# Kernel optimization log

Measured on AMD Instinct MI355X. Metric: run time of the kernel, lower is better.

Reference implementation:

```python
import jax, jax.numpy as jnp
import numpy as np
from jax import lax

B, N, D, OUT = 256, 4096, 512, 512
EPS = 1e-5
NPOINT = 128  # 4 modalities * 32 tokens each


def setup_inputs() -> dict:
    key = jax.random.key(0)
    ks = jax.random.split(key, 32)
    f32 = jnp.float32
    nrm = lambda k, s, sc=0.05: jax.random.normal(k, s, f32) * sc
    inp = {
        'rgb': jax.random.normal(ks[0], (B, 49, D), f32),
        'depth': jax.random.normal(ks[1], (B, 49, D), f32),
        'mmwave': jax.random.normal(ks[2], (B, 32, D), f32),
        'lidar': jax.random.normal(ks[3], (B, 32, D), f32),
        'lidar_points': jax.random.normal(ks[4], (B, N, 3), f32),
        # per-modality conv1d(k=1) weights, stacked [rgb, depth, mmwave, lidar]
        'conv_w': nrm(ks[5], (4, OUT, D)),
        'conv_b': nrm(ks[6], (4, OUT)),
        # eval-mode BatchNorm1d params per modality
        'bn_g': 1.0 + nrm(ks[7], (4, OUT)),
        'bn_b': nrm(ks[8], (4, OUT)),
        'bn_m': nrm(ks[9], (4, OUT)),
        'bn_v': 0.5 + jax.random.uniform(ks[10], (4, OUT), f32),
        # nn.Linear(49,32) for rgb/depth, nn.Linear(32,32) for mmwave/lidar
        'lin_w_img': nrm(ks[11], (2, 32, 49)),
        'lin_b_img': nrm(ks[12], (2, 32)),
        'lin_w_pc': nrm(ks[13], (2, 32, 32)),
        'lin_b_pc': nrm(ks[14], (2, 32)),
        # pos_enc_layer: Conv1d(3,128,1)+BN+ReLU, Conv1d(128,OUT,1)+BN+ReLU
        'pe_w1': nrm(ks[15], (128, 3)),
        'pe_b1': nrm(ks[16], (128,)),
        'pe_g1': 1.0 + nrm(ks[17], (128,)),
        'pe_bb1': nrm(ks[18], (128,)),
        'pe_m1': nrm(ks[19], (128,)),
        'pe_v1': 0.5 + jax.random.uniform(ks[20], (128,), f32),
        'pe_w2': nrm(ks[21], (OUT, 128)),
        'pe_b2': nrm(ks[22], (OUT,)),
        'pe_g2': 1.0 + nrm(ks[23], (OUT,)),
        'pe_bb2': nrm(ks[24], (OUT,)),
        'pe_m2': nrm(ks[25], (OUT,)),
        'pe_v2': 0.5 + jax.random.uniform(ks[26], (OUT,), f32),
    }
    return inp


def _bn(x, g, b, m, v):
    # x: [B, C, L]; eval-mode batchnorm over channel dim
    return (x - m[:, None]) * (g / jnp.sqrt(v + EPS))[:, None] + b[:, None]


def _branch(x, cw, cb, g, bb, m, v, lw, lb):
    # x: [B, L, D] (already the un-permuted feature); conv1d(k=1) == matmul
    h = jnp.einsum('bld,od->bol', x, cw) + cb[:, None]  # [B, OUT, L]
    h = jax.nn.relu(_bn(h, g, bb, m, v))
    h = jnp.einsum('bol,kl->bok', h, lw) + lb           # Linear on last dim -> [B, OUT, 32]
    return jax.nn.relu(h)


def _fps(xyz, npoint):
    # faithful farthest point sampling: npoint sequential iterations as lax.scan
    Bb, Nn, _ = xyz.shape
    far0 = jax.random.randint(jax.random.key(42), (Bb,), 0, Nn)
    dist0 = jnp.full((Bb, Nn), 1e10, xyz.dtype)
    def step(carry, _):
        distance, farthest = carry
        idx = jnp.broadcast_to(farthest[:, None, None], (Bb, 1, 3))
        centroid = jnp.take_along_axis(xyz, idx, axis=1)      # [B,1,3]
        d = jnp.sum((xyz - centroid) ** 2, -1)                # [B,N]
        distance = jnp.minimum(distance, d)
        return (distance, jnp.argmax(distance, -1)), farthest
    _, idxs = lax.scan(step, (dist0, far0), None, length=npoint)
    return jnp.transpose(idxs)  # [B, npoint]


def reference(rgb, depth, mmwave, lidar, lidar_points,
              conv_w, conv_b, bn_g, bn_b, bn_m, bn_v,
              lin_w_img, lin_b_img, lin_w_pc, lin_b_pc,
              pe_w1, pe_b1, pe_g1, pe_bb1, pe_m1, pe_v1,
              pe_w2, pe_b2, pe_g2, pe_bb2, pe_m2, pe_v2):
    # active_modalities = ['rgb','depth','mmwave','lidar']
    feats = [
        _branch(rgb,    conv_w[0], conv_b[0], bn_g[0], bn_b[0], bn_m[0], bn_v[0], lin_w_img[0], lin_b_img[0]),
        _branch(depth,  conv_w[1], conv_b[1], bn_g[1], bn_b[1], bn_m[1], bn_v[1], lin_w_img[1], lin_b_img[1]),
        _branch(mmwave, conv_w[2], conv_b[2], bn_g[2], bn_b[2], bn_m[2], bn_v[2], lin_w_pc[0], lin_b_pc[0]),
        _branch(lidar,  conv_w[3], conv_b[3], bn_g[3], bn_b[3], bn_m[3], bn_v[3], lin_w_pc[1], lin_b_pc[1]),
    ]
    proj = jnp.transpose(jnp.concatenate(feats, axis=2), (0, 2, 1))  # [B, 128, OUT]
    S = proj.shape[1]
    fps_idx = _fps(lidar_points, S)                                   # [B, S]
    gi = jnp.broadcast_to(fps_idx[..., None], (lidar_points.shape[0], S, 3))
    new_xyz = jnp.take_along_axis(lidar_points, gi, axis=1)           # [B, S, 3]
    h = jnp.einsum('bsd,od->bos', new_xyz, pe_w1) + pe_b1[:, None]    # [B,128,S]
    h = jax.nn.relu(_bn(h, pe_g1, pe_bb1, pe_m1, pe_v1))
    h = jnp.einsum('bcs,oc->bos', h, pe_w2) + pe_b2[:, None]          # [B,OUT,S]
    h = jax.nn.relu(_bn(h, pe_g2, pe_bb2, pe_m2, pe_v2))
    return proj + jnp.transpose(h, (0, 2, 1))
```

## Files before the change

kernel.cpp:

```cpp
#include <hip/hip_runtime.h>
#include <stdint.h>

typedef unsigned int u32;
typedef unsigned short u16;

typedef __attribute__((ext_vector_type(8))) short bf16x8;
typedef __attribute__((ext_vector_type(8))) unsigned short u16x8;
typedef __attribute__((ext_vector_type(4))) float f32x4;

__device__ __forceinline__ u16 f2bfu(float f) {
  union { float f; u32 u; } v; v.f = f;
  return (u16)((v.u + 0x7FFFu + ((v.u >> 16) & 1u)) >> 16);
}
__device__ __forceinline__ float bf2f(u16 h) {
  union { u32 u; float f; } v; v.u = ((u32)h) << 16;
  return v.f;
}

__device__ __forceinline__ void gload16(const void* g, void* l) {
  __builtin_amdgcn_global_load_lds(
      (const __attribute__((address_space(1))) void*)g,
      (__attribute__((address_space(3))) void*)l, 16, 0, 0);
}

// ... 16 lines not shown
                        x0 += x1; x1 = rotl32(x1,c); x1 ^= x0; \
                        x0 += x1; x1 = rotl32(x1,d); x1 ^= x0; }
  TF_G(13,15,26,6);  x0 += k1;  x1 += ks2 + 1u;
  TF_G(17,29,16,24); x0 += ks2; x1 += k0  + 2u;
  TF_G(13,15,26,6);  x0 += k0;  x1 += k1  + 3u;
  TF_G(17,29,16,24); x0 += k1;  x1 += ks2 + 4u;
  TF_G(13,15,26,6);  x0 += ks2; x1 += k0  + 5u;
#undef TF_G
  return make_uint2(x0, x1);
}

__global__ __launch_bounds__(256) void convert_kernel(
    const float* __restrict__ rgb, const float* __restrict__ depth,
    const float* __restrict__ mmw, const float* __restrict__ lid,
    const float* __restrict__ conv_w, u16* __restrict__ Wc, u16* __restrict__ Xc,
    const float* __restrict__ pw2,
    const float* __restrict__ pg1, const float* __restrict__ pbb1,
    const float* __restrict__ pm1, const float* __restrict__ pv1,
    const float* __restrict__ pb1,
    const float* __restrict__ pg2, const float* __restrict__ pbb2,
    const float* __restrict__ pm2, const float* __restrict__ pv2,
    const float* __restrict__ pb2,
    u16* __restrict__ W2h, u16* __restrict__ W2l,
    float* __restrict__ sc1C1, float* __restrict__ sc2C2)
{
  const int bid = blockIdx.x, tid = threadIdx.x;
  if (bid < 12288) {
    float4 v0 = make_float4(0.f, 0.f, 0.f, 0.f), v1 = v0;
    const int y = bid >> 4, ks = bid & 15;
    const int l = tid >> 2, seg = tid & 3;
    const float* xp; size_t row = 0; bool valid = true;
    if (y < 256)      { xp = rgb;   row = (size_t)y * 49 + l;         valid = (l < 49); }
    else if (y < 512) { xp = depth; row = (size_t)(y - 256) * 49 + l; valid = (l < 49); }
    else if (y < 640) { xp = mmw;   row = (size_t)(y - 512) * 64 + l; }
    else              { xp = lid;   row = (size_t)(y - 640) * 64 + l; }
    if (valid) {
      const float* s = xp + row * 512 + ks * 32 + seg * 8;
      v0 = *(const float4*)s; v1 = *(const float4*)(s + 4);
    }
    char* dst = (char*)Xc + (size_t)y * 65536 + ks * 4096 + l * 64 + ((seg ^ ((l >> 1) & 3)) << 4);
    u16x8 pk;
    pk[0] = f2bfu(v0.x); pk[1] = f2bfu(v0.y); pk[2] = f2bfu(v0.z); pk[3] = f2bfu(v0.w);
    pk[4] = f2bfu(v1.x); pk[5] = f2bfu(v1.y); pk[6] = f2bfu(v1.z); pk[7] = f2bfu(v1.w);
    *(u16x8*)dst = pk;
  } else if (bid < 12800) {
    const int t = bid - 12288;
    const int tile = t >> 1, half = t & 1;
    const int row = (tid >> 2) + half * 64, seg = tid & 3;
    const float* s = conv_w + (size_t)((tile >> 4) * 128 + row) * 512 + (tile & 15) * 32 + seg * 8;
    float4 v0 = *(const float4*)s; float4 v1 = *(const float4*)(s + 4);
    char* dst = (char*)Wc + (size_t)tile * 8192 + row * 64 + ((seg ^ ((row >> 1) & 3)) << 4);
    u16x8 pk;
    pk[0] = f2bfu(v0.x); pk[1] = f2bfu(v0.y); pk[2] = f2bfu(v0.z); pk[3] = f2bfu(v0.w);
    pk[4] = f2bfu(v1.x); pk[5] = f2bfu(v1.y); pk[6] = f2bfu(v1.z); pk[7] = f2bfu(v1.w);
    *(u16x8*)dst = pk;
  } else if (bid < 12832) {
    const int idx = (bid - 12800) * 2048 + tid * 8;
    const float* s = pw2 + idx;
    float4 v0 = *(const float4*)s; float4 v1 = *(const float4*)(s + 4);
    float vv[8] = {v0.x, v0.y, v0.z, v0.w, v1.x, v1.y, v1.z, v1.w};
    u16x8 hh, hl;
#pragma unroll
    for (int j = 0; j < 8; j++) {
      u16 hi = f2bfu(vv[j]);
      hh[j] = hi;
      hl[j] = f2bfu(vv[j] - bf2f(hi));
    }
    *(u16x8*)(W2h + idx) = hh;
    *(u16x8*)(W2l + idx) = hl;
  } else {
    if (tid < 128) {
      float sc = pg1[tid] / sqrtf(pv1[tid] + 1e-5f);
      sc1C1[tid]       = sc;
      sc1C1[128 + tid] = (pb1[tid] - pm1[tid]) * sc + pbb1[tid];
    }
    for (int o = tid; o < 512; o += 256) {
      float sc = pg2[o] / sqrtf(pv2[o] + 1e-5f);
      sc2C2[o]       = sc;
      sc2C2[512 + o] = (pb2[o] - pm2[o]) * sc + pbb2[o];
    }
  }
}

#define FSMEM_SZ 52864

__global__ __launch_bounds__(256) void fused_kernel(
    const float* __restrict__ pts, int* __restrict__ fps_idx,
    const u16* __restrict__ Wc, const u16* __restrict__ Xc,
    const float* __restrict__ conv_b,
    const float* __restrict__ bn_g, const float* __restrict__ bn_b,
    const float* __restrict__ bn_m, const float* __restrict__ bn_v,
    const float* __restrict__ lin_w_img, const float* __restrict__ lin_b_img,
    const float* __restrict__ lin_w_pc, const float* __restrict__ lin_b_pc,
    float* __restrict__ out)
{
  __shared__ __align__(16) char sm[FSMEM_SZ];
  const int tid = threadIdx.x;

  if (blockIdx.x < 256) {
    float* xs = (float*)sm;
    float* ys = (float*)(sm + 16384);
    float* zs = (float*)(sm + 32768);
    float* rv2 = (float*)(sm + 49152);
    int*   ri2 = (int*)(sm + 49184);
    const int b = blockIdx.x;
    const float* pb = pts + (size_t)b * 4096 * 3;

    __builtin_amdgcn_s_setprio(1);

    for (int i = tid; i < 12288; i += 256) {
      float v = pb[i];
      int n = i / 3, c = i - n * 3;
      float* dstp = (c == 0) ? xs : (c == 1) ? ys : zs;
      dstp[n] = v;
    }
    __syncthreads();

    float xr[16], yr[16], zr[16], dreg[16];
#pragma unroll
    for (int i = 0; i < 16; i++) {
      int n = tid + (i << 8);
      xr[i] = xs[n]; yr[i] = ys[n]; zr[i] = zs[n];
      dreg[i] = 1e10f;
    }

    uint2 k2 = threefry2x32(0u, 42u, 0u, 1u);
    uint2 r  = threefry2x32(k2.x, k2.y, 0u, (u32)b);
    int far  = (int)((r.x ^ r.y) & 4095u);
    const int wv = tid >> 6;

    for (int s = 0; s < 128; s++) {
      if (tid == 0) fps_idx[b * 128 + s] = far;
      float cx = xs[far], cy = ys[far], cz = zs[far];
      float bv[16]; int bn[16];
#pragma unroll
      for (int i = 0; i < 16; i++) {
        float dx = __fsub_rn(xr[i], cx);
        float dy = __fsub_rn(yr[i], cy);
        float dz = __fsub_rn(zr[i], cz);
        float d  = __fadd_rn(__fadd_rn(__fmul_rn(dx, dx), __fmul_rn(dy, dy)), __fmul_rn(dz, dz));
        float nd = fminf(dreg[i], d);
        dreg[i] = nd;
        bv[i] = nd; bn[i] = tid + (i << 8);
      }
#define MRG(i, j) if (bv[j] > bv[i]) { bv[i] = bv[j]; bn[i] = bn[j]; }
      MRG(0, 8)  MRG(1, 9)  MRG(2, 10) MRG(3, 11)
      MRG(4, 12) MRG(5, 13) MRG(6, 14) MRG(7, 15)
      MRG(0, 4)  MRG(1, 5)  MRG(2, 6)  MRG(3, 7)
      MRG(0, 2)  MRG(1, 3)
      MRG(0, 1)
#undef MRG
      float bestv = bv[0]; int besti = bn[0];
      dpp_merge<0x111>(bestv, besti);
      dpp_merge<0x112>(bestv, besti);
      dpp_merge<0x114>(bestv, besti);
      dpp_merge<0x118>(bestv, besti);
      dpp_merge<0x142>(bestv, besti);
      dpp_merge<0x143>(bestv, besti);
      float wbv = __int_as_float(__builtin_amdgcn_readlane(__float_as_int(bestv), 63));
      int   wbi = __builtin_amdgcn_readlane(besti, 63);

      const int par = s & 1;
      if ((tid & 63) == 0) { rv2[par * 4 + wv] = wbv; ri2[par * 4 + wv] = wbi; }
      __syncthreads();
      float bvv = rv2[par * 4]; int bii = ri2[par * 4];
#pragma unroll
      for (int w2 = 1; w2 < 4; w2++) {
        float wvv = rv2[par * 4 + w2]; int wii = ri2[par * 4 + w2];
        if (wvv > bvv || (wvv == bvv && wii < bii)) { bvv = wvv; bii = wii; }
      }
      far = bii;
    }
    return;
  }

  const int g  = (int)blockIdx.x - 256;
  const int ot = g & 3;
  const int y  = g >> 2;
  int mod, bidx = 0, bg = 0;
  if      (y < 256) { mod = 0; bidx = y; }
  else if (y < 512) { mod = 1; bidx = y - 256; }
  else if (y < 640) { mod = 2; bg   = y - 512; }
  else              { mod = 3; bg   = y - 640; }
  const bool img = (mod < 2);
  const int  L   = img ? 49 : 32;
  const float* lw = img ? (lin_w_img + mod * 32 * 49) : (lin_w_pc + (mod - 2) * 32 * 32);
  const float* lb = img ? (lin_b_img + mod * 32)      : (lin_b_pc + (mod - 2) * 32);

  u16*   lw2 = (u16*)(sm + 47104);
  float* bnA = (float*)(sm + 51712);
  float* bnC = (float*)(sm + 52224);
  float* lbs = (float*)(sm + 52736);
  u16*   hsB = (u16*)(sm + 24576);
  float* Cb  = (float*)sm;

  for (int i = tid; i < 32 * 64; i += 256) {
    int kk = i >> 6, l = i & 63;
    float v = (l < L) ? lw[kk * L + l] : 0.f;
    lw2[kk * 72 + l] = f2bfu(v);
  }
  if (tid < 32) lbs[tid] = lb[tid];
  if (tid < 128) {
    int o = mod * 512 + ot * 128 + tid;
    float sc = bn_g[o] / sqrtf(bn_v[o] + 1e-5f);
    bnA[tid] = sc;
    bnC[tid] = (conv_b[o] - bn_m[o]) * sc + bn_b[o];
  }

  const int lane = tid & 63, w = tid >> 6, quad = lane >> 4, lm = lane & 15;
  const int xorq = ((lm >> 1) & 3) << 4;
  const int soff = w * 1024 + lane * 16;

  const char* wcB = (const char*)Wc + (size_t)(mod * 4 + ot) * (16 * 8192);
  const char* xcB = (const char*)Xc + (size_t)y * 65536;

  f32x4 acc[2][4];
#pragma unroll
  for (int mi = 0; mi < 2; mi++)
#pragma unroll
    for (int nt = 0; nt < 4; nt++) acc[mi][nt] = (f32x4){0.f, 0.f, 0.f, 0.f};

  asm volatile("s_waitcnt vmcnt(0)" ::: "memory");
  gload16(wcB + soff,        sm + soff);
  gload16(wcB + soff + 4096, sm + soff + 4096);
  gload16(xcB + soff,        sm + 16384 + soff);

#pragma unroll
  for (int ks = 0; ks < 16; ks++) {
    const int cur = ks & 1;
    if (ks < 15) {
      const char* wsrc = wcB + (ks + 1) * 8192;
      const char* xsrc = xcB + (ks + 1) * 4096;
      char* wd = sm + (cur ^ 1) * 8192;
      char* xd = sm + 16384 + (cur ^ 1) * 4096;
      gload16(wsrc + soff,        wd + soff);
      gload16(wsrc + soff + 4096, wd + soff + 4096);
      gload16(xsrc + soff,        xd + soff);
      asm volatile("s_waitcnt vmcnt(3)" ::: "memory");
    } else {
      asm volatile("s_waitcnt vmcnt(0)" ::: "memory");
    }
    __builtin_amdgcn_s_barrier();
    asm volatile("" ::: "memory");
    const char* wbc = sm + cur * 8192;
    const char* xbc = sm + 16384 + cur * 4096;
    bf16x8 af[2], bfr[4];
#pragma unroll
    for (int mi = 0; mi < 2; mi++)
      af[mi] = *(const bf16x8*)(wbc + w * 2048 + mi * 1024 + lm * 64 + ((quad * 16) ^ xorq));
#pragma unroll
    for (int nt = 0; nt < 4; nt++)
      bfr[nt] = *(const bf16x8*)(xbc + nt * 1024 + lm * 64 + ((quad * 16) ^ xorq));
#pragma unroll
    for (int mi = 0; mi < 2; mi++)
#pragma unroll
      for (int nt = 0; nt < 4; nt++)
        acc[mi][nt] = __builtin_amdgcn_mfma_f32_16x16x32_bf16(af[mi], bfr[nt], acc[mi][nt], 0, 0, 0);
    asm volatile("s_waitcnt lgkmcnt(0)" ::: "memory");
    __builtin_amdgcn_s_barrier();
  }

#pragma unroll
  for (int mi = 0; mi < 2; mi++)
#pragma unroll
    for (int nt = 0; nt < 4; nt++)
#pragma unroll
      for (int r = 0; r < 4; r++) {
        int o_loc = w * 32 + mi * 16 + quad * 4 + r;
        int l     = nt * 16 + lm;
        float v = acc[mi][nt][r] * bnA[o_loc] + bnC[o_loc];
        hsB[o_loc * 88 + l] = f2bfu(v > 0.f ? v : 0.f);
      }
  __syncthreads();

  const int npass = img ? 1 : 2;
  const int nkt   = img ? 2 : 1;
  for (int p = 0; p < npass; p++) {
    f32x4 c2[2][2];
#pragma unroll
    for (int mi = 0; mi < 2; mi++)
#pragma unroll
      for (int nt2 = 0; nt2 < 2; nt2++) c2[mi][nt2] = (f32x4){0.f, 0.f, 0.f, 0.f};
    for (int kt = 0; kt < nkt; kt++) {
      int aoff = img ? kt * 32 : p * 32;
      int boff = img ? kt * 32 : 0;
      bf16x8 a2[2], b2[2];
#pragma unroll
      for (int mi = 0; mi < 2; mi++)
        a2[mi] = *(const bf16x8*)&hsB[(w * 32 + mi * 16 + lm) * 88 + aoff + quad * 8];
#pragma unroll
      for (int nt2 = 0; nt2 < 2; nt2++)
        b2[nt2] = *(const bf16x8*)&lw2[(nt2 * 16 + lm) * 72 + boff + quad * 8];
#pragma unroll
      for (int mi = 0; mi < 2; mi++)
#pragma unroll
        for (int nt2 = 0; nt2 < 2; nt2++)
          c2[mi][nt2] = __builtin_amdgcn_mfma_f32_16x16x32_bf16(a2[mi], b2[nt2], c2[mi][nt2], 0, 0, 0);
    }
#pragma unroll
    for (int mi = 0; mi < 2; mi++)
#pragma unroll
      for (int nt2 = 0; nt2 < 2; nt2++)
#pragma unroll
        for (int r = 0; r < 4; r++) {
          int kk    = nt2 * 16 + lm;
          int o_loc = w * 32 + mi * 16 + quad * 4 + r;
          float v = c2[mi][nt2][r] + lbs[kk];
          Cb[kk * 132 + o_loc] = v > 0.f ? v : 0.f;
        }
    __syncthreads();
    int b_out = img ? bidx : (bg * 2 + p);
    for (int i = tid; i < 4096; i += 256) {
      int kk = i >> 7, j = i & 127;
      out[((size_t)b_out * 128 + mod * 32 + kk) * 512 + ot * 128 + j] = Cb[kk * 132 + j];
    }
    if (p + 1 < npass) __syncthreads();
  }
}

__global__ __launch_bounds__(256) void pe_mfma_kernel(
    const float* __restrict__ pts, const int* __restrict__ fps_idx,
    const float* __restrict__ w1,
    const u16* __restrict__ W2h, const u16* __restrict__ W2l,
    const float* __restrict__ sc1C1, const float* __restrict__ sc2C2,
    float* __restrict__ out)
{
  __shared__ __align__(16) char sm[65536];
  u16* Ph = (u16*)sm;
  u16* Pl = (u16*)(sm + 16384);
  u16* Wh = (u16*)(sm + 32768);
  u16* Wl = (u16*)(sm + 49152);
  const int ot = blockIdx.x;
  const int st = blockIdx.y;
  const int b  = blockIdx.z;
  const int tid = threadIdx.x;

  for (int i = tid; i < 1024; i += 256) {
    int o = i >> 4, gn = i & 15;
    u16x8 vh = *(const u16x8*)(W2h + ((size_t)(ot * 64 + o)) * 128 + gn * 8);
    u16x8 vl = *(const u16x8*)(W2l + ((size_t)(ot * 64 + o)) * 128 + gn * 8);
    int gg = gn ^ (o & 15);
    *(u16x8*)(Wh + o * 128 + gg * 8) = vh;
    *(u16x8*)(Wl + o * 128 + gg * 8) = vl;
  }
  {
    int s_l = tid >> 2;
    int cq  = (tid & 3) * 32;
    int s   = st * 64 + s_l;
    int n   = fps_idx[b * 128 + s];
    float px = pts[((size_t)b * 4096 + n) * 3 + 0];
    float py = pts[((size_t)b * 4096 + n) * 3 + 1];
    float pz = pts[((size_t)b * 4096 + n) * 3 + 2];
    for (int c0 = 0; c0 < 32; c0 += 8) {
      u16x8 hh, hl;
#pragma unroll
      for (int j = 0; j < 8; j++) {
        int c = cq + c0 + j;
        float d = fmaf(pz, w1[c * 3 + 2], fmaf(py, w1[c * 3 + 1], px * w1[c * 3]));
        float h = d * sc1C1[c] + sc1C1[128 + c];
        h = h > 0.f ? h : 0.f;
        u16 hi = f2bfu(h);
        hh[j] = hi;
        hl[j] = f2bfu(h - bf2f(hi));
      }
      int gn = (cq + c0) >> 3;
      int gg = gn ^ (s_l & 15);
      *(u16x8*)(Ph + s_l * 128 + gg * 8) = hh;
      *(u16x8*)(Pl + s_l * 128 + gg * 8) = hl;
    }
  }
  __syncthreads();

  const int lane = tid & 63, w = tid >> 6, quad = lane >> 4, lm = lane & 15;
  f32x4 acc[4];
#pragma unroll
  for (int nt = 0; nt < 4; nt++) acc[nt] = (f32x4){0.f, 0.f, 0.f, 0.f};

  const int arow = w * 16 + lm;
#pragma unroll
  for (int kt = 0; kt < 4; kt++) {
    int ag = ((kt * 4 + quad) ^ (arow & 15)) * 8;
    bf16x8 pah = *(const bf16x8*)(Ph + arow * 128 + ag);
    bf16x8 pal = *(const bf16x8*)(Pl + arow * 128 + ag);
#pragma unroll
    for (int nt = 0; nt < 4; nt++) {
      int brow = nt * 16 + lm;
      int bg = ((kt * 4 + quad) ^ (brow & 15)) * 8;
      bf16x8 wbh = *(const bf16x8*)(Wh + brow * 128 + bg);
      bf16x8 wbl = *(const bf16x8*)(Wl + brow * 128 + bg);
      acc[nt] = __builtin_amdgcn_mfma_f32_16x16x32_bf16(pah, wbh, acc[nt], 0, 0, 0);
      acc[nt] = __builtin_amdgcn_mfma_f32_16x16x32_bf16(pah, wbl, acc[nt], 0, 0, 0);
      acc[nt] = __builtin_amdgcn_mfma_f32_16x16x32_bf16(pal, wbh, acc[nt], 0, 0, 0);
    }
  }

#pragma unroll
  for (int nt = 0; nt < 4; nt++) {
    int o = ot * 64 + nt * 16 + lm;
    float sc = sc2C2[o], C = sc2C2[512 + o];
#pragma unroll
    for (int r = 0; r < 4; r++) {
      int s = st * 64 + w * 16 + quad * 4 + r;
      float v = acc[nt][r] * sc + C;
      v = v > 0.f ? v : 0.f;
      size_t oi = ((size_t)b * 128 + s) * 512 + o;
      out[oi] = out[oi] + v;
    }
  }
}

#define WB_OFF   0
#define XB_OFF   8192
#define CB_OFF   0
#define HS_OFF   16896
#define LW2_OFF  39424
#define BNA_OFF  44032
#define BNC_OFF  44544
#define LBS_OFF  45056
#define SMEM_SZ  45184

__global__ __launch_bounds__(256) void branch_kernel(
    const float* __restrict__ x0p, const float* __restrict__ x1p,
    const float* __restrict__ x2p, const float* __restrict__ x3p,
    const float* __restrict__ conv_w, const float* __restrict__ conv_b,
    const float* __restrict__ bn_g, const float* __restrict__ bn_b,
    const float* __restrict__ bn_m, const float* __restrict__ bn_v,
    const float* __restrict__ lin_w_img, const float* __restrict__ lin_b_img,
    const float* __restrict__ lin_w_pc, const float* __restrict__ lin_b_pc,
    float* __restrict__ out)
{
  __shared__ __align__(16) char sm[SMEM_SZ];
  u16*   Wb  = (u16*)(sm + WB_OFF);
  u16*   Xb  = (u16*)(sm + XB_OFF);
  float* Cb  = (float*)(sm + CB_OFF);
  u16*   hsB = (u16*)(sm + HS_OFF);
  u16*   lw2 = (u16*)(sm + LW2_OFF);
  float* bnA = (float*)(sm + BNA_OFF);
  float* bnC = (float*)(sm + BNC_OFF);
  float* lbs = (float*)(sm + LBS_OFF);

  const int ot  = blockIdx.x;
  const int tid = threadIdx.x;
  int y = blockIdx.y;
  int mod, bidx = 0, bg = 0;
  if      (y < 256) { mod = 0; bidx = y; }
  else if (y < 512) { mod = 1; bidx = y - 256; }
  else if (y < 640) { mod = 2; bg   = y - 512; }
  else              { mod = 3; bg   = y - 640; }
  const bool img = (mod < 2);
  const int  L   = img ? 49 : 32;
  const float* xp = (mod == 0) ? x0p : (mod == 1) ? x1p : (mod == 2) ? x2p : x3p;
  const float* lw = img ? (lin_w_img + mod * 32 * 49) : (lin_w_pc + (mod - 2) * 32 * 32);
  const float* lb = img ? (lin_b_img + mod * 32)      : (lin_b_pc + (mod - 2) * 32);

  for (int i = tid; i < 32 * 64; i += 256) {
    int kk = i >> 6, l = i & 63;
    float v = (l < L) ? lw[kk * L + l] : 0.f;
    lw2[kk * 72 + l] = f2bfu(v);
  }
  if (tid < 32) lbs[tid] = lb[tid];
  if (tid < 128) {
    int o = mod * 512 + ot * 128 + tid;
    float sc = bn_g[o] / sqrtf(bn_v[o] + 1e-5f);
    bnA[tid] = sc;
    bnC[tid] = (conv_b[o] - bn_m[o]) * sc + bn_b[o];
  }

  const int lane = tid & 63, w = tid >> 6, quad = lane >> 4, lm = lane & 15;
  const float* wbase = conv_w + (size_t)(mod * 512 + ot * 128) * 512;

  f32x4 acc[2][4];
#pragma unroll
  for (int mi = 0; mi < 2; mi++)
#pragma unroll
    for (int nt = 0; nt < 4; nt++) acc[mi][nt] = (f32x4){0.f, 0.f, 0.f, 0.f};

  for (int ks = 0; ks < 16; ks++) {
    int k0 = ks * 32;
    __syncthreads();
    for (int i = tid; i < 1024; i += 256) {
      int row = i >> 3, seg = i & 7;
      float4 v = *(const float4*)(wbase + (size_t)row * 512 + k0 + seg * 4);
      u16* d = &Wb[row * 32 + seg * 4];
      d[0] = f2bfu(v.x); d[1] = f2bfu(v.y); d[2] = f2bfu(v.z); d[3] = f2bfu(v.w);
    }
    for (int i = tid; i < 512; i += 256) {
      int l = i >> 3, seg = i & 7;
      float4 v = make_float4(0.f, 0.f, 0.f, 0.f);
      if (img) {
        if (l < 49) v = *(const float4*)(xp + (size_t)(bidx * 49 + l) * 512 + k0 + seg * 4);
      } else {
// ... 182 lines not shown
    }
  }
  __syncthreads();

  const int tx = tid & 15, ty = tid >> 4;
  float acc[4][4];
#pragma unroll
  for (int j = 0; j < 4; j++)
#pragma unroll
    for (int i = 0; i < 4; i++) acc[j][i] = 0.f;

  for (int c = 0; c < 128; c += 4) {
    float4 wv[4];
#pragma unroll
    for (int j = 0; j < 4; j++) wv[j] = *(const float4*)&w2s[tx + 16 * j][c];
#pragma unroll
    for (int si = 0; si < 4; si++) {
      float4 hv = *(const float4*)&h1T[ty + 16 * si][c];
#pragma unroll
      for (int j = 0; j < 4; j++) {
        acc[j][si] = fmaf(hv.x, wv[j].x, acc[j][si]);
        acc[j][si] = fmaf(hv.y, wv[j].y, acc[j][si]);
        acc[j][si] = fmaf(hv.z, wv[j].z, acc[j][si]);
        acc[j][si] = fmaf(hv.w, wv[j].w, acc[j][si]);
      }
    }
  }

#pragma unroll
  for (int j = 0; j < 4; j++) {
    int o = ot * 64 + tx + 16 * j;
    float sc = g2[o] / sqrtf(v2[o] + 1e-5f);
    float C  = (b2[o] - m2[o]) * sc + bb2[o];
#pragma unroll
    for (int si = 0; si < 4; si++) {
      int s = st * 64 + ty + 16 * si;
      float v = acc[j][si] * sc + C;
      v = v > 0.f ? v : 0.f;
      size_t oi = ((size_t)b * 128 + s) * 512 + o;
      out[oi] = out[oi] + v;
    }
  }
}

extern "C" void kernel_launch(void* const* d_in, const int* in_sizes, int n_in,
                              void* d_out, int out_size, void* d_ws, size_t ws_size,
                              hipStream_t stream) {
  const float* rgb    = (const float*)d_in[0];
  const float* depth  = (const float*)d_in[1];
  const float* mmwave = (const float*)d_in[2];
  const float* lidar  = (const float*)d_in[3];
  const float* pts    = (const float*)d_in[4];
  const float* conv_w = (const float*)d_in[5];
  const float* conv_b = (const float*)d_in[6];
  const float* bn_g   = (const float*)d_in[7];
  const float* bn_b   = (const float*)d_in[8];
  const float* bn_m   = (const float*)d_in[9];
  const float* bn_v   = (const float*)d_in[10];
  const float* lwi    = (const float*)d_in[11];
  const float* lbi    = (const float*)d_in[12];
  const float* lwp    = (const float*)d_in[13];
  const float* lbp    = (const float*)d_in[14];
  const float* pw1    = (const float*)d_in[15];
  const float* pb1    = (const float*)d_in[16];
  const float* pg1    = (const float*)d_in[17];
  const float* pbb1   = (const float*)d_in[18];
  const float* pm1    = (const float*)d_in[19];
  const float* pv1    = (const float*)d_in[20];
  const float* pw2    = (const float*)d_in[21];
  const float* pb2    = (const float*)d_in[22];
  const float* pg2    = (const float*)d_in[23];
  const float* pbb2   = (const float*)d_in[24];
  const float* pm2    = (const float*)d_in[25];
  const float* pv2    = (const float*)d_in[26];
  float* out = (float*)d_out;
  int* fps_idx = (int*)d_ws;

  const size_t O_WC   = 131072;
  const size_t O_XC   = 2228224;
  const size_t O_W2H  = 52559872;
  const size_t O_W2L  = 52690944;
  const size_t O_SC1  = 52822016;
  const size_t O_SC2  = 52823040;
  const size_t NEED   = 52827136;
  if (ws_size >= NEED) {
    u16*   Wc    = (u16*)((char*)d_ws + O_WC);
    u16*   Xc    = (u16*)((char*)d_ws + O_XC);
    u16*   W2h   = (u16*)((char*)d_ws + O_W2H);
    u16*   W2l   = (u16*)((char*)d_ws + O_W2L);
    float* sc1C1 = (float*)((char*)d_ws + O_SC1);
    float* sc2C2 = (float*)((char*)d_ws + O_SC2);
    convert_kernel<<<dim3(12833), 256, 0, stream>>>(rgb, depth, mmwave, lidar,
        conv_w, Wc, Xc, pw2, pg1, pbb1, pm1, pv1, pb1, pg2, pbb2, pm2, pv2, pb2,
        W2h, W2l, sc1C1, sc2C2);
    fused_kernel<<<dim3(3328), 256, 0, stream>>>(pts, fps_idx, Wc, Xc,
        conv_b, bn_g, bn_b, bn_m, bn_v, lwi, lbi, lwp, lbp, out);
    pe_mfma_kernel<<<dim3(8, 2, 256), 256, 0, stream>>>(pts, fps_idx, pw1,
        W2h, W2l, sc1C1, sc2C2, out);
  } else {
    branch_kernel<<<dim3(4, 768), 256, 0, stream>>>(rgb, depth, mmwave, lidar,
        conv_w, conv_b, bn_g, bn_b, bn_m, bn_v, lwi, lbi, lwp, lbp, out);
    fps_kernel<<<dim3(256), 256, 0, stream>>>(pts, fps_idx);
    pe_kernel<<<dim3(8, 2, 256), 256, 0, stream>>>(pts, fps_idx, pw1, pb1, pg1, pbb1, pm1, pv1,
        pw2, pb2, pg2, pbb2, pm2, pv2, out);
  }
}
```

Before: 430.0 us.

## Split FPS out of fused kernel and run PE before branch with fused add

Moves farthest-point sampling out of the combined kernel into its own launch, and drops the FPS-block priority hint. When the workspace is large enough, the positional-encoding MLP now runs first and writes to a scratch buffer. The branch kernel then adds that buffer while writing the final output, replacing the read-modify-write on out. This gives up the overlap of the serial FPS loop with the branch GEMMs and adds a 64MB scratch write and read, in exchange for removing the output RMW pass.

```diff
diff --git a/kernel.cpp b/kernel.cpp
--- a/kernel.cpp
+++ b/kernel.cpp
@@ -122,101 +122,98 @@
   }
 }
 
+__global__ __launch_bounds__(256) void fps2_kernel(const float* __restrict__ pts,
+                                                   int* __restrict__ fps_idx)
+{
+  __shared__ __align__(16) char sm[49216];
+  float* xs = (float*)sm;
+  float* ys = (float*)(sm + 16384);
+  float* zs = (float*)(sm + 32768);
+  float* rv2 = (float*)(sm + 49152);
+  int*   ri2 = (int*)(sm + 49184);
+  const int b = blockIdx.x, tid = threadIdx.x;
+  const float* pb = pts + (size_t)b * 4096 * 3;
+
+  for (int i = tid; i < 12288; i += 256) {
+    float v = pb[i];
+    int n = i / 3, c = i - n * 3;
+    float* dstp = (c == 0) ? xs : (c == 1) ? ys : zs;
+    dstp[n] = v;
+  }
+  __syncthreads();
+
+  float xr[16], yr[16], zr[16], dreg[16];
+#pragma unroll
+  for (int i = 0; i < 16; i++) {
+    int n = tid + (i << 8);
+    xr[i] = xs[n]; yr[i] = ys[n]; zr[i] = zs[n];
+    dreg[i] = 1e10f;
+  }
+
+  uint2 k2 = threefry2x32(0u, 42u, 0u, 1u);
+  uint2 r  = threefry2x32(k2.x, k2.y, 0u, (u32)b);
+  int far  = (int)((r.x ^ r.y) & 4095u);
+  const int wv = tid >> 6;
+
+  for (int s = 0; s < 128; s++) {
+    if (tid == 0) fps_idx[b * 128 + s] = far;
+    float cx = xs[far], cy = ys[far], cz = zs[far];
+    float bv[16]; int bn[16];
+#pragma unroll
+    for (int i = 0; i < 16; i++) {
+      float dx = __fsub_rn(xr[i], cx);
+      float dy = __fsub_rn(yr[i], cy);
+      float dz = __fsub_rn(zr[i], cz);
+      float d  = __fadd_rn(__fadd_rn(__fmul_rn(dx, dx), __fmul_rn(dy, dy)), __fmul_rn(dz, dz));
+      float nd = fminf(dreg[i], d);
+      dreg[i] = nd;
+      bv[i] = nd; bn[i] = tid + (i << 8);
+    }
+#define MRG(i, j) if (bv[j] > bv[i]) { bv[i] = bv[j]; bn[i] = bn[j]; }
+    MRG(0, 8)  MRG(1, 9)  MRG(2, 10) MRG(3, 11)
+    MRG(4, 12) MRG(5, 13) MRG(6, 14) MRG(7, 15)
+    MRG(0, 4)  MRG(1, 5)  MRG(2, 6)  MRG(3, 7)
+    MRG(0, 2)  MRG(1, 3)
+    MRG(0, 1)
+#undef MRG
+    float bestv = bv[0]; int besti = bn[0];
+    dpp_merge<0x111>(bestv, besti);
+    dpp_merge<0x112>(bestv, besti);
+    dpp_merge<0x114>(bestv, besti);
+    dpp_merge<0x118>(bestv, besti);
+    dpp_merge<0x142>(bestv, besti);
+    dpp_merge<0x143>(bestv, besti);
+    float wbv = __int_as_float(__builtin_amdgcn_readlane(__float_as_int(bestv), 63));
+    int   wbi = __builtin_amdgcn_readlane(besti, 63);
+
+    const int par = s & 1;
+    if ((tid & 63) == 0) { rv2[par * 4 + wv] = wbv; ri2[par * 4 + wv] = wbi; }
+    __syncthreads();
+    float bvv = rv2[par * 4]; int bii = ri2[par * 4];
+#pragma unroll
+    for (int w2 = 1; w2 < 4; w2++) {
+      float wvv = rv2[par * 4 + w2]; int wii = ri2[par * 4 + w2];
+      if (wvv > bvv || (wvv == bvv && wii < bii)) { bvv = wvv; bii = wii; }
+    }
+    far = bii;
+  }
+}
+
 #define FSMEM_SZ 52864
 
-__global__ __launch_bounds__(256) void fused_kernel(
-    const float* __restrict__ pts, int* __restrict__ fps_idx,
+__global__ __launch_bounds__(256) void branch2_kernel(
     const u16* __restrict__ Wc, const u16* __restrict__ Xc,
     const float* __restrict__ conv_b,
     const float* __restrict__ bn_g, const float* __restrict__ bn_b,
     const float* __restrict__ bn_m, const float* __restrict__ bn_v,
     const float* __restrict__ lin_w_img, const float* __restrict__ lin_b_img,
     const float* __restrict__ lin_w_pc, const float* __restrict__ lin_b_pc,
-    float* __restrict__ out)
+    const float* __restrict__ peY, float* __restrict__ out)
 {
   __shared__ __align__(16) char sm[FSMEM_SZ];
   const int tid = threadIdx.x;
-
-  if (blockIdx.x < 256) {
-    float* xs = (float*)sm;
-    float* ys = (float*)(sm + 16384);
-    float* zs = (float*)(sm + 32768);
-    float* rv2 = (float*)(sm + 49152);
-    int*   ri2 = (int*)(sm + 49184);
-    const int b = blockIdx.x;
-    const float* pb = pts + (size_t)b * 4096 * 3;
-
-    __builtin_amdgcn_s_setprio(1);
-
-    for (int i = tid; i < 12288; i += 256) {
-      float v = pb[i];
-      int n = i / 3, c = i - n * 3;
-      float* dstp = (c == 0) ? xs : (c == 1) ? ys : zs;
-      dstp[n] = v;
-    }
-    __syncthreads();
-
-    float xr[16], yr[16], zr[16], dreg[16];
-#pragma unroll
-    for (int i = 0; i < 16; i++) {
-      int n = tid + (i << 8);
-      xr[i] = xs[n]; yr[i] = ys[n]; zr[i] = zs[n];
-      dreg[i] = 1e10f;
-    }
-
-    uint2 k2 = threefry2x32(0u, 42u, 0u, 1u);
-    uint2 r  = threefry2x32(k2.x, k2.y, 0u, (u32)b);
-    int far  = (int)((r.x ^ r.y) & 4095u);
-    const int wv = tid >> 6;
-
-    for (int s = 0; s < 128; s++) {
-      if (tid == 0) fps_idx[b * 128 + s] = far;
-      float cx = xs[far], cy = ys[far], cz = zs[far];
-      float bv[16]; int bn[16];
-#pragma unroll
-      for (int i = 0; i < 16; i++) {
-        float dx = __fsub_rn(xr[i], cx);
-        float dy = __fsub_rn(yr[i], cy);
-        float dz = __fsub_rn(zr[i], cz);
-        float d  = __fadd_rn(__fadd_rn(__fmul_rn(dx, dx), __fmul_rn(dy, dy)), __fmul_rn(dz, dz));
-        float nd = fminf(dreg[i], d);
-        dreg[i] = nd;
-        bv[i] = nd; bn[i] = tid + (i << 8);
-      }
-#define MRG(i, j) if (bv[j] > bv[i]) { bv[i] = bv[j]; bn[i] = bn[j]; }
-      MRG(0, 8)  MRG(1, 9)  MRG(2, 10) MRG(3, 11)
-      MRG(4, 12) MRG(5, 13) MRG(6, 14) MRG(7, 15)
-      MRG(0, 4)  MRG(1, 5)  MRG(2, 6)  MRG(3, 7)
-      MRG(0, 2)  MRG(1, 3)
-      MRG(0, 1)
-#undef MRG
-      float bestv = bv[0]; int besti = bn[0];
-      dpp_merge<0x111>(bestv, besti);
-      dpp_merge<0x112>(bestv, besti);
-      dpp_merge<0x114>(bestv, besti);
-      dpp_merge<0x118>(bestv, besti);
-      dpp_merge<0x142>(bestv, besti);
-      dpp_merge<0x143>(bestv, besti);
-      float wbv = __int_as_float(__builtin_amdgcn_readlane(__float_as_int(bestv), 63));
-      int   wbi = __builtin_amdgcn_readlane(besti, 63);
-
-      const int par = s & 1;
-      if ((tid & 63) == 0) { rv2[par * 4 + wv] = wbv; ri2[par * 4 + wv] = wbi; }
-      __syncthreads();
-      float bvv = rv2[par * 4]; int bii = ri2[par * 4];
-#pragma unroll
-      for (int w2 = 1; w2 < 4; w2++) {
-        float wvv = rv2[par * 4 + w2]; int wii = ri2[par * 4 + w2];
-        if (wvv > bvv || (wvv == bvv && wii < bii)) { bvv = wvv; bii = wii; }
-      }
-      far = bii;
-    }
-    return;
-  }
-
-  const int g  = (int)blockIdx.x - 256;
-  const int ot = g & 3;
-  const int y  = g >> 2;
+  const int ot = blockIdx.x;
+  const int y  = blockIdx.y;
   int mod, bidx = 0, bg = 0;
   if      (y < 256) { mod = 0; bidx = y; }
   else if (y < 512) { mod = 1; bidx = y - 256; }
@@ -350,20 +347,29 @@
         }
     __syncthreads();
     int b_out = img ? bidx : (bg * 2 + p);
-    for (int i = tid; i < 4096; i += 256) {
-      int kk = i >> 7, j = i & 127;
-      out[((size_t)b_out * 128 + mod * 32 + kk) * 512 + ot * 128 + j] = Cb[kk * 132 + j];
+    if (peY != nullptr) {
+      const float* pe = peY + ((size_t)b_out * 128 + mod * 32) * 512 + ot * 128;
+      for (int i = tid; i < 4096; i += 256) {
+        int kk = i >> 7, j = i & 127;
+        out[((size_t)b_out * 128 + mod * 32 + kk) * 512 + ot * 128 + j] =
+            Cb[kk * 132 + j] + pe[(size_t)kk * 512 + j];
+      }
+    } else {
+      for (int i = tid; i < 4096; i += 256) {
+        int kk = i >> 7, j = i & 127;
+        out[((size_t)b_out * 128 + mod * 32 + kk) * 512 + ot * 128 + j] = Cb[kk * 132 + j];
+      }
     }
     if (p + 1 < npass) __syncthreads();
   }
 }
 
-__global__ __launch_bounds__(256) void pe_mfma_kernel(
+__device__ __forceinline__ void pe_body(
     const float* __restrict__ pts, const int* __restrict__ fps_idx,
     const float* __restrict__ w1,
     const u16* __restrict__ W2h, const u16* __restrict__ W2l,
     const float* __restrict__ sc1C1, const float* __restrict__ sc2C2,
-    float* __restrict__ out)
+    float* __restrict__ dst, bool rmw)
 {
   __shared__ __align__(16) char sm[65536];
   u16* Ph = (u16*)sm;
@@ -444,9 +450,30 @@
       float v = acc[nt][r] * sc + C;
       v = v > 0.f ? v : 0.f;
       size_t oi = ((size_t)b * 128 + s) * 512 + o;
-      out[oi] = out[oi] + v;
-    }
-  }
+      if (rmw) dst[oi] = dst[oi] + v;
+      else     dst[oi] = v;
+    }
+  }
+}
+
+__global__ __launch_bounds__(256) void peg_kernel(
+    const float* __restrict__ pts, const int* __restrict__ fps_idx,
+    const float* __restrict__ w1,
+    const u16* __restrict__ W2h, const u16* __restrict__ W2l,
+    const float* __restrict__ sc1C1, const float* __restrict__ sc2C2,
+    float* __restrict__ peY)
+{
+  pe_body(pts, fps_idx, w1, W2h, W2l, sc1C1, sc2C2, peY, false);
+}
+
+__global__ __launch_bounds__(256) void pe_mfma_kernel(
+    const float* __restrict__ pts, const int* __restrict__ fps_idx,
+    const float* __restrict__ w1,
+    const u16* __restrict__ W2h, const u16* __restrict__ W2l,
+    const float* __restrict__ sc1C1, const float* __restrict__ sc2C2,
+    float* __restrict__ out)
+{
+  pe_body(pts, fps_idx, w1, W2h, W2l, sc1C1, sc2C2, out, true);
 }
 
 #define WB_OFF   0
@@ -795,8 +822,11 @@
   const size_t O_W2L  = 52690944;
   const size_t O_SC1  = 52822016;
   const size_t O_SC2  = 52823040;
-  const size_t NEED   = 52827136;
-  if (ws_size >= NEED) {
+  const size_t O_PEY  = 52827136;
+  const size_t NEED_MID = 52827136;
+  const size_t NEED_BIG = O_PEY + (size_t)256 * 128 * 512 * 4;
+
+  if (ws_size >= NEED_MID) {
     u16*   Wc    = (u16*)((char*)d_ws + O_WC);
     u16*   Xc    = (u16*)((char*)d_ws + O_XC);
     u16*   W2h   = (u16*)((char*)d_ws + O_W2H);
@@ -806,10 +836,19 @@
     convert_kernel<<<dim3(12833), 256, 0, stream>>>(rgb, depth, mmwave, lidar,
         conv_w, Wc, Xc, pw2, pg1, pbb1, pm1, pv1, pb1, pg2, pbb2, pm2, pv2, pb2,
         W2h, W2l, sc1C1, sc2C2);
-    fused_kernel<<<dim3(3328), 256, 0, stream>>>(pts, fps_idx, Wc, Xc,
-        conv_b, bn_g, bn_b, bn_m, bn_v, lwi, lbi, lwp, lbp, out);
-    pe_mfma_kernel<<<dim3(8, 2, 256), 256, 0, stream>>>(pts, fps_idx, pw1,
-        W2h, W2l, sc1C1, sc2C2, out);
+    fps2_kernel<<<dim3(256), 256, 0, stream>>>(pts, fps_idx);
+    if (ws_size >= NEED_BIG) {
+      float* peY = (float*)((char*)d_ws + O_PEY);
+      peg_kernel<<<dim3(8, 2, 256), 256, 0, stream>>>(pts, fps_idx, pw1,
+          W2h, W2l, sc1C1, sc2C2, peY);
+      branch2_kernel<<<dim3(4, 768), 256, 0, stream>>>(Wc, Xc,
+          conv_b, bn_g, bn_b, bn_m, bn_v, lwi, lbi, lwp, lbp, peY, out);
+    } else {
+      branch2_kernel<<<dim3(4, 768), 256, 0, stream>>>(Wc, Xc,
+          conv_b, bn_g, bn_b, bn_m, bn_v, lwi, lbi, lwp, lbp, nullptr, out);
+      pe_mfma_kernel<<<dim3(8, 2, 256), 256, 0, stream>>>(pts, fps_idx, pw1,
+          W2h, W2l, sc1C1, sc2C2, out);
+    }
   } else {
     branch_kernel<<<dim3(4, 768), 256, 0, stream>>>(rgb, depth, mmwave, lidar,
         conv_w, conv_b, bn_g, bn_b, bn_m, bn_v, lwi, lbi, lwp, lbp, out);
```

Result: slower. 478.4 us (+11.3%).

## Split FPS out of fused kernel, widen FPS to 512 threads, batch PE per sample

Applied to the files above, without the earlier changes.

Pulls the farthest-point-sampling blocks out of the combined branch/FPS launch into a separate kernel that uses 512 threads per batch, so each thread handles 8 points instead of 16. The branch work now runs alone in its own grid. The positional-encoding kernel is restructured to one block per batch: it builds the full 128x128 hidden tile in LDS once and reads W2 fragments directly from global memory rather than staging them in LDS. The cost is that FPS no longer overlaps with the branch GEMMs, since they now run back to back in separate launches, and W2 reads come from global/L2.

```diff
diff --git a/kernel.cpp b/kernel.cpp
--- a/kernel.cpp
+++ b/kernel.cpp
@@ -122,10 +122,84 @@
   }
 }
 
+__global__ __launch_bounds__(512, 1) void fps3_kernel(const float* __restrict__ pts,
+                                                      int* __restrict__ fps_idx)
+{
+  __shared__ __align__(16) char sm[49280];
+  float* xs = (float*)sm;
+  float* ys = (float*)(sm + 16384);
+  float* zs = (float*)(sm + 32768);
+  float* rv2 = (float*)(sm + 49152);
+  int*   ri2 = (int*)(sm + 49216);
+  const int b = blockIdx.x, tid = threadIdx.x;
+  const float* pb = pts + (size_t)b * 4096 * 3;
+
+  for (int i = tid; i < 12288; i += 512) {
+    float v = pb[i];
+    int n = i / 3, c = i - n * 3;
+    float* dstp = (c == 0) ? xs : (c == 1) ? ys : zs;
+    dstp[n] = v;
+  }
+  __syncthreads();
+
+  float xr[8], yr[8], zr[8], dreg[8];
+#pragma unroll
+  for (int i = 0; i < 8; i++) {
+    int n = tid + (i << 9);
+    xr[i] = xs[n]; yr[i] = ys[n]; zr[i] = zs[n];
+    dreg[i] = 1e10f;
+  }
+
+  uint2 k2 = threefry2x32(0u, 42u, 0u, 1u);
+  uint2 r  = threefry2x32(k2.x, k2.y, 0u, (u32)b);
+  int far  = (int)((r.x ^ r.y) & 4095u);
+  const int wv = tid >> 6;
+
+  for (int s = 0; s < 128; s++) {
+    if (tid == 0) fps_idx[b * 128 + s] = far;
+    float cx = xs[far], cy = ys[far], cz = zs[far];
+    float bv[8]; int bn[8];
+#pragma unroll
+    for (int i = 0; i < 8; i++) {
+      float dx = __fsub_rn(xr[i], cx);
+      float dy = __fsub_rn(yr[i], cy);
+      float dz = __fsub_rn(zr[i], cz);
+      float d  = __fadd_rn(__fadd_rn(__fmul_rn(dx, dx), __fmul_rn(dy, dy)), __fmul_rn(dz, dz));
+      float nd = fminf(dreg[i], d);
+      dreg[i] = nd;
+      bv[i] = nd; bn[i] = tid + (i << 9);
+    }
+#define MRG(i, j) if (bv[j] > bv[i]) { bv[i] = bv[j]; bn[i] = bn[j]; }
+    MRG(0, 4) MRG(1, 5) MRG(2, 6) MRG(3, 7)
+    MRG(0, 2) MRG(1, 3)
+    MRG(0, 1)
+#undef MRG
+    float bestv = bv[0]; int besti = bn[0];
+    dpp_merge<0x111>(bestv, besti);
+    dpp_merge<0x112>(bestv, besti);
+    dpp_merge<0x114>(bestv, besti);
+    dpp_merge<0x118>(bestv, besti);
+    dpp_merge<0x142>(bestv, besti);
+    dpp_merge<0x143>(bestv, besti);
+    float wbv = __int_as_float(__builtin_amdgcn_readlane(__float_as_int(bestv), 63));
+    int   wbi = __builtin_amdgcn_readlane(besti, 63);
+
+    const int par = s & 1;
+    if ((tid & 63) == 0) { rv2[par * 8 + wv] = wbv; ri2[par * 8 + wv] = wbi; }
+    __syncthreads();
+    float bvv = rv2[par * 8]; int bii = ri2[par * 8];
+#pragma unroll
+    for (int w2 = 1; w2 < 8; w2++) {
+      float wvv = rv2[par * 8 + w2]; int wii = ri2[par * 8 + w2];
+      if (wvv > bvv || (wvv == bvv && wii < bii)) { bvv = wvv; bii = wii; }
+    }
+    far = bii;
+  }
+}
+
 #define FSMEM_SZ 52864
 
-__global__ __launch_bounds__(256) void fused_kernel(
-    const float* __restrict__ pts, int* __restrict__ fps_idx,
+__global__ __launch_bounds__(256) void branch2_kernel(
     const u16* __restrict__ Wc, const u16* __restrict__ Xc,
     const float* __restrict__ conv_b,
     const float* __restrict__ bn_g, const float* __restrict__ bn_b,
@@ -136,87 +210,8 @@
 {
   __shared__ __align__(16) char sm[FSMEM_SZ];
   const int tid = threadIdx.x;
-
-  if (blockIdx.x < 256) {
-    float* xs = (float*)sm;
-    float* ys = (float*)(sm + 16384);
-    float* zs = (float*)(sm + 32768);
-    float* rv2 = (float*)(sm + 49152);
-    int*   ri2 = (int*)(sm + 49184);
-    const int b = blockIdx.x;
-    const float* pb = pts + (size_t)b * 4096 * 3;
-
-    __builtin_amdgcn_s_setprio(1);
-
-    for (int i = tid; i < 12288; i += 256) {
-      float v = pb[i];
-      int n = i / 3, c = i - n * 3;
-      float* dstp = (c == 0) ? xs : (c == 1) ? ys : zs;
-      dstp[n] = v;
-    }
-    __syncthreads();
-
-    float xr[16], yr[16], zr[16], dreg[16];
-#pragma unroll
-    for (int i = 0; i < 16; i++) {
-      int n = tid + (i << 8);
-      xr[i] = xs[n]; yr[i] = ys[n]; zr[i] = zs[n];
-      dreg[i] = 1e10f;
-    }
-
-    uint2 k2 = threefry2x32(0u, 42u, 0u, 1u);
-    uint2 r  = threefry2x32(k2.x, k2.y, 0u, (u32)b);
-    int far  = (int)((r.x ^ r.y) & 4095u);
-    const int wv = tid >> 6;
-
-    for (int s = 0; s < 128; s++) {
-      if (tid == 0) fps_idx[b * 128 + s] = far;
-      float cx = xs[far], cy = ys[far], cz = zs[far];
-      float bv[16]; int bn[16];
-#pragma unroll
-      for (int i = 0; i < 16; i++) {
-        float dx = __fsub_rn(xr[i], cx);
-        float dy = __fsub_rn(yr[i], cy);
-        float dz = __fsub_rn(zr[i], cz);
-        float d  = __fadd_rn(__fadd_rn(__fmul_rn(dx, dx), __fmul_rn(dy, dy)), __fmul_rn(dz, dz));
-        float nd = fminf(dreg[i], d);
-        dreg[i] = nd;
-        bv[i] = nd; bn[i] = tid + (i << 8);
-      }
-#define MRG(i, j) if (bv[j] > bv[i]) { bv[i] = bv[j]; bn[i] = bn[j]; }
-      MRG(0, 8)  MRG(1, 9)  MRG(2, 10) MRG(3, 11)
-      MRG(4, 12) MRG(5, 13) MRG(6, 14) MRG(7, 15)
-      MRG(0, 4)  MRG(1, 5)  MRG(2, 6)  MRG(3, 7)
-      MRG(0, 2)  MRG(1, 3)
-      MRG(0, 1)
-#undef MRG
-      float bestv = bv[0]; int besti = bn[0];
-      dpp_merge<0x111>(bestv, besti);
-      dpp_merge<0x112>(bestv, besti);
-      dpp_merge<0x114>(bestv, besti);
-      dpp_merge<0x118>(bestv, besti);
-      dpp_merge<0x142>(bestv, besti);
-      dpp_merge<0x143>(bestv, besti);
-      float wbv = __int_as_float(__builtin_amdgcn_readlane(__float_as_int(bestv), 63));
-      int   wbi = __builtin_amdgcn_readlane(besti, 63);
-
-      const int par = s & 1;
-      if ((tid & 63) == 0) { rv2[par * 4 + wv] = wbv; ri2[par * 4 + wv] = wbi; }
-      __syncthreads();
-      float bvv = rv2[par * 4]; int bii = ri2[par * 4];
-#pragma unroll
-      for (int w2 = 1; w2 < 4; w2++) {
-        float wvv = rv2[par * 4 + w2]; int wii = ri2[par * 4 + w2];
-        if (wvv > bvv || (wvv == bvv && wii < bii)) { bvv = wvv; bii = wii; }
-      }
-      far = bii;
-    }
-    return;
-  }
-
-  const int g  = (int)blockIdx.x - 256;
-  const int ot = g & 3;
-  const int y  = g >> 2;
+  const int ot = blockIdx.x;
+  const int y  = blockIdx.y;
   int mod, bidx = 0, bg = 0;
   if      (y < 256) { mod = 0; bidx = y; }
   else if (y < 512) { mod = 1; bidx = y - 256; }
@@ -358,53 +353,45 @@
   }
 }
 
-__global__ __launch_bounds__(256) void pe_mfma_kernel(
+__global__ __launch_bounds__(256, 1) void pe_batch_kernel(
     const float* __restrict__ pts, const int* __restrict__ fps_idx,
     const float* __restrict__ w1,
     const u16* __restrict__ W2h, const u16* __restrict__ W2l,
     const float* __restrict__ sc1C1, const float* __restrict__ sc2C2,
     float* __restrict__ out)
 {
-  __shared__ __align__(16) char sm[65536];
-  u16* Ph = (u16*)sm;
-  u16* Pl = (u16*)(sm + 16384);
-  u16* Wh = (u16*)(sm + 32768);
-  u16* Wl = (u16*)(sm + 49152);
-  const int ot = blockIdx.x;
-  const int st = blockIdx.y;
-  const int b  = blockIdx.z;
-  const int tid = threadIdx.x;
-
-  for (int i = tid; i < 1024; i += 256) {
-    int o = i >> 4, gn = i & 15;
-    u16x8 vh = *(const u16x8*)(W2h + ((size_t)(ot * 64 + o)) * 128 + gn * 8);
-    u16x8 vl = *(const u16x8*)(W2l + ((size_t)(ot * 64 + o)) * 128 + gn * 8);
-    int gg = gn ^ (o & 15);
-    *(u16x8*)(Wh + o * 128 + gg * 8) = vh;
-    *(u16x8*)(Wl + o * 128 + gg * 8) = vl;
-  }
+  __shared__ __align__(16) char sm[68096];
+  u16*   Ph  = (u16*)sm;
+  u16*   Pl  = (u16*)(sm + 32768);
+  float* w1s = (float*)(sm + 65536);
+  float* sc1 = (float*)(sm + 67072);
+  const int b = blockIdx.x, tid = threadIdx.x;
+
+  for (int i = tid; i < 384; i += 256) w1s[i] = w1[i];
+  if (tid < 256) sc1[tid] = sc1C1[tid];
+  __syncthreads();
+
   {
-    int s_l = tid >> 2;
-    int cq  = (tid & 3) * 32;
-    int s   = st * 64 + s_l;
-    int n   = fps_idx[b * 128 + s];
+    int s_l = tid >> 1;
+    int half = (tid & 1) * 64;
+    int n = fps_idx[b * 128 + s_l];
     float px = pts[((size_t)b * 4096 + n) * 3 + 0];
     float py = pts[((size_t)b * 4096 + n) * 3 + 1];
     float pz = pts[((size_t)b * 4096 + n) * 3 + 2];
-    for (int c0 = 0; c0 < 32; c0 += 8) {
+    for (int c0 = 0; c0 < 64; c0 += 8) {
       u16x8 hh, hl;
 #pragma unroll
       for (int j = 0; j < 8; j++) {
-        int c = cq + c0 + j;
-        float d = fmaf(pz, w1[c * 3 + 2], fmaf(py, w1[c * 3 + 1], px * w1[c * 3]));
-        float h = d * sc1C1[c] + sc1C1[128 + c];
+        int c = half + c0 + j;
+        float d = fmaf(pz, w1s[c * 3 + 2], fmaf(py, w1s[c * 3 + 1], px * w1s[c * 3]));
+        float h = d * sc1[c] + sc1[128 + c];
         h = h > 0.f ? h : 0.f;
         u16 hi = f2bfu(h);
         hh[j] = hi;
         hl[j] = f2bfu(h - bf2f(hi));
       }
-      int gn = (cq + c0) >> 3;
-      int gg = gn ^ (s_l & 15);
+      int g  = (half + c0) >> 3;
+      int gg = g ^ (s_l & 15);
       *(u16x8*)(Ph + s_l * 128 + gg * 8) = hh;
       *(u16x8*)(Pl + s_l * 128 + gg * 8) = hl;
     }
@@ -412,39 +399,41 @@
   __syncthreads();
 
   const int lane = tid & 63, w = tid >> 6, quad = lane >> 4, lm = lane & 15;
-  f32x4 acc[4];
-#pragma unroll
-  for (int nt = 0; nt < 4; nt++) acc[nt] = (f32x4){0.f, 0.f, 0.f, 0.f};
-
-  const int arow = w * 16 + lm;
-#pragma unroll
-  for (int kt = 0; kt < 4; kt++) {
-    int ag = ((kt * 4 + quad) ^ (arow & 15)) * 8;
-    bf16x8 pah = *(const bf16x8*)(Ph + arow * 128 + ag);
-    bf16x8 pal = *(const bf16x8*)(Pl + arow * 128 + ag);
-#pragma unroll
-    for (int nt = 0; nt < 4; nt++) {
-      int brow = nt * 16 + lm;
-      int bg = ((kt * 4 + quad) ^ (brow & 15)) * 8;
-      bf16x8 wbh = *(const bf16x8*)(Wh + brow * 128 + bg);
-      bf16x8 wbl = *(const bf16x8*)(Wl + brow * 128 + bg);
-      acc[nt] = __builtin_amdgcn_mfma_f32_16x16x32_bf16(pah, wbh, acc[nt], 0, 0, 0);
-      acc[nt] = __builtin_amdgcn_mfma_f32_16x16x32_bf16(pah, wbl, acc[nt], 0, 0, 0);
-      acc[nt] = __builtin_amdgcn_mfma_f32_16x16x32_bf16(pal, wbh, acc[nt], 0, 0, 0);
-    }
-  }
-
-#pragma unroll
-  for (int nt = 0; nt < 4; nt++) {
-    int o = ot * 64 + nt * 16 + lm;
-    float sc = sc2C2[o], C = sc2C2[512 + o];
-#pragma unroll
-    for (int r = 0; r < 4; r++) {
-      int s = st * 64 + w * 16 + quad * 4 + r;
-      float v = acc[nt][r] * sc + C;
-      v = v > 0.f ? v : 0.f;
-      size_t oi = ((size_t)b * 128 + s) * 512 + o;
-      out[oi] = out[oi] + v;
+  const u16* W2hB = W2h + (size_t)w * 128 * 128;
+  const u16* W2lB = W2l + (size_t)w * 128 * 128;
+
+  for (int st2 = 0; st2 < 8; st2++) {
+    bf16x8 Ah[4], Al[4];
+    const int srow = st2 * 16 + lm;
+#pragma unroll
+    for (int kt = 0; kt < 4; kt++) {
+      int ag = ((kt * 4 + quad) ^ (srow & 15)) * 8;
+      Ah[kt] = *(const bf16x8*)(Ph + srow * 128 + ag);
+      Al[kt] = *(const bf16x8*)(Pl + srow * 128 + ag);
+    }
+#pragma unroll
+    for (int ot2 = 0; ot2 < 8; ot2++) {
+      f32x4 a = (f32x4){0.f, 0.f, 0.f, 0.f};
+      const u16* bh = W2hB + (ot2 * 16 + lm) * 128 + quad * 8;
+      const u16* bl = W2lB + (ot2 * 16 + lm) * 128 + quad * 8;
+#pragma unroll
+      for (int kt = 0; kt < 4; kt++) {
+        bf16x8 Bh = *(const bf16x8*)(bh + kt * 32);
+        bf16x8 Bl = *(const bf16x8*)(bl + kt * 32);
+        a = __builtin_amdgcn_mfma_f32_16x16x32_bf16(Ah[kt], Bh, a, 0, 0, 0);
+        a = __builtin_amdgcn_mfma_f32_16x16x32_bf16(Ah[kt], Bl, a, 0, 0, 0);
+        a = __builtin_amdgcn_mfma_f32_16x16x32_bf16(Al[kt], Bh, a, 0, 0, 0);
+      }
+      int o = w * 128 + ot2 * 16 + lm;
+      float sc = sc2C2[o], C = sc2C2[512 + o];
+#pragma unroll
+      for (int r = 0; r < 4; r++) {
+        int s = st2 * 16 + quad * 4 + r;
+        float v = a[r] * sc + C;
+        v = v > 0.f ? v : 0.f;
+        size_t oi = ((size_t)b * 128 + s) * 512 + o;
+        out[oi] = out[oi] + v;
+      }
     }
   }
 }
@@ -796,6 +785,7 @@
   const size_t O_SC1  = 52822016;
   const size_t O_SC2  = 52823040;
   const size_t NEED   = 52827136;
+
   if (ws_size >= NEED) {
     u16*   Wc    = (u16*)((char*)d_ws + O_WC);
     u16*   Xc    = (u16*)((char*)d_ws + O_XC);
@@ -806,9 +796,10 @@
     convert_kernel<<<dim3(12833), 256, 0, stream>>>(rgb, depth, mmwave, lidar,
         conv_w, Wc, Xc, pw2, pg1, pbb1, pm1, pv1, pb1, pg2, pbb2, pm2, pv2, pb2,
         W2h, W2l, sc1C1, sc2C2);
-    fused_kernel<<<dim3(3328), 256, 0, stream>>>(pts, fps_idx, Wc, Xc,
+    branch2_kernel<<<dim3(4, 768), 256, 0, stream>>>(Wc, Xc,
         conv_b, bn_g, bn_b, bn_m, bn_v, lwi, lbi, lwp, lbp, out);
-    pe_mfma_kernel<<<dim3(8, 2, 256), 256, 0, stream>>>(pts, fps_idx, pw1,
+    fps3_kernel<<<dim3(256), 512, 0, stream>>>(pts, fps_idx);
+    pe_batch_kernel<<<dim3(256), 256, 0, stream>>>(pts, fps_idx, pw1,
         W2h, W2l, sc1C1, sc2C2, out);
   } else {
     branch_kernel<<<dim3(4, 768), 256, 0, stream>>>(rgb, depth, mmwave, lidar,
```

Result: slower. 486.6 us (+13.2%).
